# Performance work log

Hardware: AMD Instinct MI355X
Metric: run time of the kernel (lower is better)

Reference implementation:

```python
import jax, jax.numpy as jnp
import numpy as np

B, S, HID, NH = 4, 4096, 1024, 16
D = HID // NH
EPS = 1e-5


def setup_inputs() -> dict:
    key = jax.random.key(0)
    ks = jax.random.split(key, 8)
    x = jax.random.normal(ks[0], (B, S, HID), dtype=jnp.float32)
    sc = 0.03  # ~xavier for 1024x1024
    Wq = jax.random.normal(ks[1], (HID, HID), dtype=jnp.float32) * sc
    Wk = jax.random.normal(ks[2], (HID, HID), dtype=jnp.float32) * sc
    Wv = jax.random.normal(ks[3], (HID, HID), dtype=jnp.float32) * sc
    Wbeta = jax.random.normal(ks[4], (HID, NH), dtype=jnp.float32) * sc
    b_beta = jnp.full((NH,), 0.9, dtype=jnp.float32)  # init.constant_(0.9)
    Wo = jax.random.normal(ks[5], (HID, HID), dtype=jnp.float32) * sc
    b_o = jnp.zeros((HID,), dtype=jnp.float32)
    ln_g = jnp.ones((HID,), dtype=jnp.float32)
    ln_b = jnp.zeros((HID,), dtype=jnp.float32)
    return {"x": x, "Wq": Wq, "Wk": Wk, "Wv": Wv, "Wbeta": Wbeta,
            "b_beta": b_beta, "Wo": Wo, "b_o": b_o, "ln_g": ln_g, "ln_b": ln_b}


def _delta_scan(q, k, v, beta):
    # q,k,v: (B,S,NH,D); beta: (B,S,NH)
    # Faithful to torch einsum 'bik,bji->bjk' with broadcast over i:
    # update[b,h,:,k'] = k_t[b,h,k'] * sum_d v_t[b,h,d]  (same row repeated)
    vsum = v.sum(-1)  # (B,S,NH)
    qs = jnp.moveaxis(q, 1, 0)       # (S,B,NH,D)
    ks_ = jnp.moveaxis(k, 1, 0)
    vs = jnp.moveaxis(vsum, 1, 0)    # (S,B,NH)
    bs = jnp.moveaxis(beta, 1, 0)    # (S,B,NH)

    def step(h, inp):
        q_t, k_t, vsum_t, beta_t = inp
        h = h * beta_t[..., None, None]
        h = h + (k_t * vsum_t[..., None])[:, :, None, :]  # broadcast over rows
        o_t = jnp.einsum('bhj,bhjk->bhk', q_t, h)
        return h, o_t

    h0 = jnp.zeros((q.shape[0], q.shape[2], D, D), dtype=q.dtype)
    _, o = jax.lax.scan(step, h0, (qs, ks_, vs, bs))
    return jnp.moveaxis(o, 0, 1)  # (B,S,NH,D)


def reference(x, Wq, Wk, Wv, Wbeta, b_beta, Wo, b_o, ln_g, ln_b):
    b, s, hid = x.shape
    residual = x
    q = (x @ Wq).reshape(b, s, NH, D)
    k = (x @ Wk).reshape(b, s, NH, D)
    v = (x @ Wv).reshape(b, s, NH, D)
    beta = jax.nn.sigmoid(x @ Wbeta + b_beta)  # (B,S,NH)
    o = _delta_scan(q, k, v, beta).reshape(b, s, hid)
    out = o @ Wo + b_o  # dropout is identity in eval
    y = residual + out
    mu = y.mean(-1, keepdims=True)
    var = ((y - mu) ** 2).mean(-1, keepdims=True)
    return ln_g * (y - mu) * jax.lax.rsqrt(var + EPS) + ln_b
```

## Files before the change

kernel.cpp:

```cpp
#include <hip/hip_runtime.h>
#include <hip/hip_bf16.h>

typedef unsigned short u16;
typedef unsigned int   u32;
typedef u32 __attribute__((address_space(1))) gas_u32;
typedef u32 __attribute__((address_space(3))) las_u32;
typedef __bf16 bf16x8 __attribute__((ext_vector_type(8)));
typedef float  f32x4  __attribute__((ext_vector_type(4)));

constexpr int BATCH = 4, SEQ = 4096, HID = 1024, NH = 16, DH = 64;
constexpr int M  = BATCH * SEQ;
constexpr int KD = HID;

__device__ __forceinline__ u16 f2bf(float f) {
  __hip_bfloat16 h = __float2bfloat16(f);
  u16 u; __builtin_memcpy(&u, &h, 2); return u;
}
__device__ __forceinline__ float bf2f(u16 u) {
  u32 x = ((u32)u) << 16; float f; __builtin_memcpy(&f, &x, 4); return f;
}


__global__ __launch_bounds__(256) void transpose_cast(const float* __restrict__ Wk,
                                                      const float* __restrict__ Wo,
                                                      u16* __restrict__ WkT,
                                                      u16* __restrict__ WoT) {
  __shared__ float tile[32][33];
  const float* src = blockIdx.z ? Wo : Wk;
  u16* dst = blockIdx.z ? WoT : WkT;
  int bx = blockIdx.x * 32, by = blockIdx.y * 32;
  int tx = threadIdx.x & 31, ty = threadIdx.x >> 5;
#pragma unroll
  for (int i = 0; i < 4; i++)
    tile[ty + i * 8][tx] = src[(size_t)(by + ty + i * 8) * HID + bx + tx];
  __syncthreads();
#pragma unroll
  for (int i = 0; i < 4; i++)
    dst[(size_t)(bx + ty + i * 8) * HID + by + tx] = f2bf(tile[tx][ty + i * 8]);
}

__global__ __launch_bounds__(256) void build_wsum(const float* __restrict__ Wq,
                                                  const float* __restrict__ Wv,
                                                  const float* __restrict__ Wbeta,
                                                  u16* __restrict__ WsT) {
  int tid = blockIdx.x * 256 + threadIdx.x;
  int c = tid >> 10, kk = tid & 1023;
  float s = 0.f;
  if (c < 16)      { for (int d = 0; d < DH; d++) s += Wq[(size_t)kk * HID + c * DH + d]; }
  else if (c < 32) { for (int d = 0; d < DH; d++) s += Wv[(size_t)kk * HID + (c - 16) * DH + d]; }
  else if (c < 48) { s = Wbeta[(size_t)kk * NH + (c - 32)]; }
  WsT[(size_t)c * HID + kk] = f2bf(s);
}

__global__ __launch_bounds__(256) void skinny_part(
    const float* __restrict__ x, const u16* __restrict__ Bt,
    float* __restrict__ pq, float* __restrict__ pv, float* __restrict__ pb,
    u16* __restrict__ xb) {
  constexpr int BM = 64, BK = 64, KC = 256;
  __shared__ u16 As[BM * BK];
  __shared__ u16 Bs[64 * BK];
  const int tid = threadIdx.x, wave = tid >> 6, lane = tid & 63;
  const int bm = (int)blockIdx.x >> 2, kc = (int)blockIdx.x & 3;
  const int k0 = kc * KC;
  const int r16 = lane & 15, hi = lane >> 4;
  const int rsub = lane >> 3, csub = (lane & 7) * 8;
  f32x4 acc[4] = {};
  const float* Ab = x + (size_t)bm * BM * KD;
  u16* xbb = xb + (size_t)bm * BM * KD;

  for (int kt = k0; kt < k0 + KC; kt += BK) {
#pragma unroll
    for (int i = 0; i < 2; i++) {
      int slot = wave * 2 + i;
      const u16* g = Bt + (size_t)(slot * 8 + rsub) * KD + kt + csub;
      __builtin_amdgcn_global_load_lds((const gas_u32*)g, (las_u32*)(Bs + slot * 512), 16, 0, 0);
    }
#pragma unroll
    for (int p = 0; p < 2; p++) {
      const int row = p * 32 + (tid >> 3);
      const int c8 = (tid & 7) * 8;
      const float4 u0 = *(const float4*)(Ab + (size_t)row * KD + kt + c8);
      const float4 u1 = *(const float4*)(Ab + (size_t)row * KD + kt + c8 + 4);
      uint4 w;
      w.x = (u32)f2bf(u0.x) | ((u32)f2bf(u0.y) << 16);
      w.y = (u32)f2bf(u0.z) | ((u32)f2bf(u0.w) << 16);
      w.z = (u32)f2bf(u1.x) | ((u32)f2bf(u1.y) << 16);
      w.w = (u32)f2bf(u1.z) | ((u32)f2bf(u1.w) << 16);
      *(uint4*)(As + row * BK + c8) = w;
      *(uint4*)(xbb + (size_t)row * KD + kt + c8) = w;
    }
    __syncthreads();
#pragma unroll
    for (int kk = 0; kk < 2; kk++) {
      bf16x8 af = *(const bf16x8*)(As + (wave * 16 + r16) * BK + kk * 32 + hi * 8);
#pragma unroll
      for (int fn = 0; fn < 4; fn++) {
        bf16x8 bfr = *(const bf16x8*)(Bs + (fn * 16 + r16) * BK + kk * 32 + hi * 8);
        acc[fn] = __builtin_amdgcn_mfma_f32_16x16x32_bf16(af, bfr, acc[fn], 0, 0, 0);
      }
    }
    __syncthreads();
  }

  const size_t kcoff = (size_t)kc * 64 * SEQ;
#pragma unroll
  for (int fn = 0; fn < 4; fn++) {
    const int col = fn * 16 + r16;
#pragma unroll
    for (int j = 0; j < 4; j++) {
      const int row = bm * BM + wave * 16 + hi * 4 + j;
      const int b = row >> 12, t = row & 4095;
      float v = acc[fn][j];
      if (col < 16)      pq[kcoff + ((size_t)(b * 16 + col)) * SEQ + t] = v;
      else if (col < 32) pv[kcoff + ((size_t)(b * 16 + col - 16)) * SEQ + t] = v;
      else if (col < 48) pb[kcoff + ((size_t)(b * 16 + col - 32)) * SEQ + t] = v;
    }
  }
}


__device__ __forceinline__ void stage_quarter(const u16* __restrict__ Gk,
                                              int q, u16* lds_tile, int tid, int wave) {
  const int row = q * 64 + (tid >> 3);
  const int s = tid & 7;
  const u16* g = Gk + (size_t)row * KD + (size_t)((s ^ (row & 7)) << 3);
  u16* l = lds_tile + q * 4096 + wave * 512;
  __builtin_amdgcn_global_load_lds((const gas_u32*)g, (las_u32*)l, 16, 0, 0);
}

__device__ __forceinline__ const bf16x8* lds_frag(const u16* lds_tile, int row, int cg) {
  return (const bf16x8*)(lds_tile + ((size_t)row << 6) + (size_t)((cg ^ (row & 7)) << 3));
}

template <int EPI>
__global__ __launch_bounds__(512) void gemm256(
    const u16* __restrict__ A, const u16* __restrict__ Bt, int N,
    u16* __restrict__ Cb, const u16* __restrict__ xres, const float* __restrict__ bias) {
  constexpr int BK = 64, NT = KD / BK;
  __shared__ u16 lds[2][2][16384];
  const int tid = threadIdx.x, wave = tid >> 6, lane = tid & 63;
  const int wm = wave >> 2, wn = wave & 3;
  const int r16 = lane & 15, hi = lane >> 4;
  const int bid = (int)blockIdx.x;
  const int bm = (bid & 7) + 8 * (bid >> 5);
  const int bn = (bid >> 3) & 3;
  const u16* Abase = A + (size_t)bm * 256 * KD;
  const u16* Bbase = Bt + (size_t)bn * 256 * KD;

  f32x4 acc[8][4] = {};

  {
    u16* la = &lds[0][0][0]; u16* lb = &lds[0][1][0];
    stage_quarter(Abase, 0, la, tid, wave);
    stage_quarter(Abase, 2, la, tid, wave);
    stage_quarter(Bbase, 0, lb, tid, wave);
    stage_quarter(Bbase, 1, lb, tid, wave);
    stage_quarter(Bbase, 2, lb, tid, wave);
    stage_quarter(Bbase, 3, lb, tid, wave);
    stage_quarter(Abase, 1, la, tid, wave);
    stage_quarter(Abase, 3, la, tid, wave);
  }
  asm volatile("s_waitcnt vmcnt(2)" ::: "memory");
  __builtin_amdgcn_s_barrier();

  for (int kt = 0; kt < NT - 1; ++kt) {
    const int cur = kt & 1;
    const u16* la = &lds[cur][0][0];
    const u16* lb = &lds[cur][1][0];
    u16* na = &lds[cur ^ 1][0][0];
    u16* nb = &lds[cur ^ 1][1][0];
    const u16* An = Abase + (kt + 1) * BK;
    const u16* Bn = Bbase + (kt + 1) * BK;

    stage_quarter(An, 0, na, tid, wave);
    stage_quarter(An, 2, na, tid, wave);
    bf16x8 bF[4][2], aF0[4][2];
#pragma unroll
    for (int kk = 0; kk < 2; ++kk) {
#pragma unroll
      for (int f = 0; f < 4; ++f)
        aF0[f][kk] = *lds_frag(la, wm * 128 + f * 16 + r16, kk * 4 + hi);
#pragma unroll
      for (int g = 0; g < 4; ++g)
        bF[g][kk] = *lds_frag(lb, wn * 64 + g * 16 + r16, kk * 4 + hi);
    }
    stage_quarter(Bn, 0, nb, tid, wave);
    stage_quarter(Bn, 1, nb, tid, wave);
    __builtin_amdgcn_s_setprio(1);
#pragma unroll
    for (int kk = 0; kk < 2; ++kk)
#pragma unroll
      for (int f = 0; f < 4; ++f)
#pragma unroll
        for (int g = 0; g < 4; ++g)
          acc[f][g] = __builtin_amdgcn_mfma_f32_16x16x32_bf16(
              aF0[f][kk], bF[g][kk], acc[f][g], 0, 0, 0);
    __builtin_amdgcn_s_setprio(0);
    asm volatile("s_waitcnt vmcnt(4)" ::: "memory");
    __builtin_amdgcn_s_barrier();

    stage_quarter(Bn, 2, nb, tid, wave);
    stage_quarter(Bn, 3, nb, tid, wave);
    bf16x8 aF1[4][2];
#pragma unroll
    for (int kk = 0; kk < 2; ++kk)
#pragma unroll
      for (int f = 0; f < 4; ++f)
        aF1[f][kk] = *lds_frag(la, wm * 128 + 64 + f * 16 + r16, kk * 4 + hi);
    stage_quarter(An, 1, na, tid, wave);
    stage_quarter(An, 3, na, tid, wave);
    __builtin_amdgcn_s_setprio(1);
#pragma unroll
    for (int kk = 0; kk < 2; ++kk)
#pragma unroll
      for (int f = 0; f < 4; ++f)
#pragma unroll
        for (int g = 0; g < 4; ++g)
          acc[4 + f][g] = __builtin_amdgcn_mfma_f32_16x16x32_bf16(
              aF1[f][kk], bF[g][kk], acc[4 + f][g], 0, 0, 0);
    __builtin_amdgcn_s_setprio(0);
    asm volatile("s_waitcnt vmcnt(2)" ::: "memory");
    __builtin_amdgcn_s_barrier();
  }

  {
    const u16* la = &lds[(NT - 1) & 1][0][0];
    const u16* lb = &lds[(NT - 1) & 1][1][0];
    bf16x8 bF[4][2], aF0[4][2];
#pragma unroll
    for (int kk = 0; kk < 2; ++kk) {
#pragma unroll
      for (int f = 0; f < 4; ++f)
        aF0[f][kk] = *lds_frag(la, wm * 128 + f * 16 + r16, kk * 4 + hi);
#pragma unroll
      for (int g = 0; g < 4; ++g)
        bF[g][kk] = *lds_frag(lb, wn * 64 + g * 16 + r16, kk * 4 + hi);
    }
    __builtin_amdgcn_s_setprio(1);
#pragma unroll
    for (int kk = 0; kk < 2; ++kk)
#pragma unroll
      for (int f = 0; f < 4; ++f)
#pragma unroll
        for (int g = 0; g < 4; ++g)
          acc[f][g] = __builtin_amdgcn_mfma_f32_16x16x32_bf16(
              aF0[f][kk], bF[g][kk], acc[f][g], 0, 0, 0);
    __builtin_amdgcn_s_setprio(0);
    asm volatile("s_waitcnt vmcnt(0)" ::: "memory");
    __builtin_amdgcn_s_barrier();
    bf16x8 aF1[4][2];
#pragma unroll
    for (int kk = 0; kk < 2; ++kk)
#pragma unroll
      for (int f = 0; f < 4; ++f)
        aF1[f][kk] = *lds_frag(la, wm * 128 + 64 + f * 16 + r16, kk * 4 + hi);
    __builtin_amdgcn_s_setprio(1);
#pragma unroll
    for (int kk = 0; kk < 2; ++kk)
#pragma unroll
      for (int f = 0; f < 4; ++f)
#pragma unroll
        for (int g = 0; g < 4; ++g)
          acc[4 + f][g] = __builtin_amdgcn_mfma_f32_16x16x32_bf16(
              aF1[f][kk], bF[g][kk], acc[4 + f][g], 0, 0, 0);
    __builtin_amdgcn_s_setprio(0);
  }

#pragma unroll
  for (int fm = 0; fm < 8; ++fm) {
#pragma unroll
    for (int fn = 0; fn < 4; ++fn) {
      const int col = bn * 256 + wn * 64 + fn * 16 + r16;
#pragma unroll
      for (int j = 0; j < 4; ++j) {
        const int row = bm * 256 + wm * 128 + fm * 16 + hi * 4 + j;
        float v = acc[fm][fn][j];
        if constexpr (EPI == 2) v += bf2f(xres[(size_t)row * N + col]) + bias[col];
        Cb[(size_t)row * N + col] = f2bf(v);
      }
    }
  }
}


__global__ __launch_bounds__(256) void scan_chunks(const u16* __restrict__ kbuf,
                                                   const float* __restrict__ pv,
                                                   const float* __restrict__ pb,
                                                   const float* __restrict__ bbeta,
                                                   float* __restrict__ Pbuf,
                                                   float* __restrict__ Rloc) {
  constexpr size_t STR = (size_t)64 * SEQ;
  const int wave = threadIdx.x >> 6, lane = threadIdx.x & 63;
  const int gid = blockIdx.x * 4 + wave;
  const int seq = gid >> 6, chunk = gid & 63;
  const int b = seq >> 4, h = seq & 15;
  const int t0 = chunk * 64;
  const size_t idx = (size_t)seq * SEQ + t0 + lane;
  const float zb = pb[idx] + pb[idx + STR] + pb[idx + 2 * STR] + pb[idx + 3 * STR] + bbeta[h];
  const float bet = 1.f / (1.f + __expf(-zb));
  const float vs  = pv[idx] + pv[idx + STR] + pv[idx + 2 * STR] + pv[idx + 3 * STR];
  const u16* kp = kbuf + ((size_t)(b * SEQ + t0)) * HID + h * DH + lane;
  float r = 0.f, P = 1.f;
#pragma unroll
  for (int tt = 0; tt < 64; tt += 8) {
    u16 kr[8];
#pragma unroll
    for (int j = 0; j < 8; j++) kr[j] = kp[(size_t)(tt + j) * HID];
#pragma unroll
    for (int j = 0; j < 8; j++) {
      float bt = __shfl(bet, tt + j);
      float vt = __shfl(vs, tt + j);
      r = fmaf(r, bt, bf2f(kr[j]) * vt);
      P *= bt;
    }
  }
  Rloc[(size_t)gid * 64 + lane] = r;
  if (lane == 0) Pbuf[gid] = P;
}

__global__ __launch_bounds__(64) void scan_prefix(const float* __restrict__ Pbuf,
                                                  const float* __restrict__ Rloc,
                                                  float* __restrict__ Rin) {
  const int seq = blockIdx.x, lane = threadIdx.x;
  const float* pp = Pbuf + seq * 64;
  const float* rl = Rloc + (size_t)seq * 64 * 64 + lane;
  float* ri = Rin + (size_t)seq * 64 * 64 + lane;
  float rin = 0.f;
#pragma unroll
  for (int c0 = 0; c0 < 64; c0 += 8) {
    float P[8], L[8];
#pragma unroll
    for (int j = 0; j < 8; j++) { P[j] = pp[c0 + j]; L[j] = rl[(size_t)(c0 + j) * 64]; }
#pragma unroll
    for (int j = 0; j < 8; j++) {
      ri[(size_t)(c0 + j) * 64] = rin;
      rin = fmaf(P[j], rin, L[j]);
    }
  }
}

__global__ __launch_bounds__(256) void scan_apply(const u16* __restrict__ kbuf,
                                                  const float* __restrict__ pq,
                                                  const float* __restrict__ pv,
                                                  const float* __restrict__ pb,
                                                  const float* __restrict__ bbeta,
                                                  const float* __restrict__ Rin,
                                                  u16* __restrict__ obuf) {
  constexpr size_t STR = (size_t)64 * SEQ;
  const int wave = threadIdx.x >> 6, lane = threadIdx.x & 63;
  const int gid = blockIdx.x * 4 + wave;
  const int seq = gid >> 6, chunk = gid & 63;
  const int b = seq >> 4, h = seq & 15;
  const int t0 = chunk * 64;
  const size_t idx = (size_t)seq * SEQ + t0 + lane;
  const float zb = pb[idx] + pb[idx + STR] + pb[idx + 2 * STR] + pb[idx + 3 * STR] + bbeta[h];
  const float bet = 1.f / (1.f + __expf(-zb));
  const float vs  = pv[idx] + pv[idx + STR] + pv[idx + 2 * STR] + pv[idx + 3 * STR];
  const float qs  = pq[idx] + pq[idx + STR] + pq[idx + 2 * STR] + pq[idx + 3 * STR];
  const u16* kp = kbuf + ((size_t)(b * SEQ + t0)) * HID + h * DH + lane;
  u16* op = obuf + ((size_t)(b * SEQ + t0)) * HID + h * DH + lane;
  float r = Rin[(size_t)gid * 64 + lane];
#pragma unroll
  for (int tt = 0; tt < 64; tt += 8) {
    u16 kr[8];
#pragma unroll
    for (int j = 0; j < 8; j++) kr[j] = kp[(size_t)(tt + j) * HID];
#pragma unroll
    for (int j = 0; j < 8; j++) {
      float bt = __shfl(bet, tt + j);
      float vt = __shfl(vs, tt + j);
      float qt = __shfl(qs, tt + j);
      r = fmaf(r, bt, bf2f(kr[j]) * vt);
      op[(size_t)(tt + j) * HID] = f2bf(qt * r);
    }
  }
}

__global__ __launch_bounds__(256) void ln_kernel(const u16* __restrict__ y,
                                                 const float* __restrict__ g,
                                                 const float* __restrict__ bt,
                                                 float* __restrict__ out) {
  const int row = blockIdx.x;
  const u16* yr = y + (size_t)row * HID;
  const int t = threadIdx.x;
  ushort4 u = *(const ushort4*)(yr + t * 4);
  float v0 = bf2f(u.x), v1 = bf2f(u.y), v2 = bf2f(u.z), v3 = bf2f(u.w);
  float s  = v0 + v1 + v2 + v3;
  float ss = v0 * v0 + v1 * v1 + v2 * v2 + v3 * v3;
#pragma unroll
  for (int m = 1; m < 64; m <<= 1) { s += __shfl_xor(s, m); ss += __shfl_xor(ss, m); }
  __shared__ float red[8];
  const int wave = t >> 6, lane = t & 63;
  if (lane == 0) { red[wave] = s; red[4 + wave] = ss; }
  __syncthreads();
  float st  = red[0] + red[1] + red[2] + red[3];
  float sst = red[4] + red[5] + red[6] + red[7];
  float mu  = st * (1.f / 1024.f);
  float var = sst * (1.f / 1024.f) - mu * mu;
  float inv = rsqrtf(var + 1e-5f);
  const int c = t * 4;
  float4 o;
  o.x = g[c + 0] * ((v0 - mu) * inv) + bt[c + 0];
  o.y = g[c + 1] * ((v1 - mu) * inv) + bt[c + 1];
  o.z = g[c + 2] * ((v2 - mu) * inv) + bt[c + 2];
  o.w = g[c + 3] * ((v3 - mu) * inv) + bt[c + 3];
  *(float4*)(out + (size_t)row * HID + c) = o;
}

extern "C" void kernel_launch(void* const* d_in, const int* in_sizes, int n_in,
                              void* d_out, int out_size, void* d_ws, size_t ws_size,
                              hipStream_t stream) {
  const float* x     = (const float*)d_in[0];
  const float* Wq    = (const float*)d_in[1];
  const float* Wk    = (const float*)d_in[2];
  const float* Wv    = (const float*)d_in[3];
  const float* Wbeta = (const float*)d_in[4];
  const float* bbeta = (const float*)d_in[5];
  const float* Wo    = (const float*)d_in[6];
  const float* b_o   = (const float*)d_in[7];
  const float* ln_g  = (const float*)d_in[8];
  const float* ln_b  = (const float*)d_in[9];
  float* out = (float*)d_out;

  char* ws = (char*)d_ws;
  size_t off = 0;
  auto alloc = [&](size_t bytes) {
    char* p = ws + off; off += (bytes + 255) & ~(size_t)255; return p;
  };
  u16* xb   = (u16*)alloc((size_t)M * HID * 2);
  u16* kbuf = (u16*)alloc((size_t)M * HID * 2);
  u16* obuf = (u16*)alloc((size_t)M * HID * 2);
  u16* WkT  = (u16*)alloc((size_t)HID * HID * 2);
  u16* WoT  = (u16*)alloc((size_t)HID * HID * 2);
  u16* WsT  = (u16*)alloc((size_t)64 * HID * 2);
  float* pq = (float*)alloc((size_t)4 * 64 * SEQ * 4);
  float* pv = (float*)alloc((size_t)4 * 64 * SEQ * 4);
  float* pb = (float*)alloc((size_t)4 * 64 * SEQ * 4);
  float* Pbuf = (float*)alloc((size_t)4096 * 4);
  float* Rloc = (float*)alloc((size_t)4096 * 64 * 4);
  float* Rin  = (float*)alloc((size_t)4096 * 64 * 4);
  u16* ybuf = kbuf;

  transpose_cast<<<dim3(32, 32, 2), 256, 0, stream>>>(Wk, Wo, WkT, WoT);
  build_wsum<<<256, 256, 0, stream>>>(Wq, Wv, Wbeta, WsT);

  skinny_part<<<(M / 64) * 4, 256, 0, stream>>>(x, WsT, pq, pv, pb, xb);

  gemm256<0><<<(M / 256) * (HID / 256), 512, 0, stream>>>(
      xb, WkT, HID, kbuf, nullptr, nullptr);

  scan_chunks<<<1024, 256, 0, stream>>>(kbuf, pv, pb, bbeta, Pbuf, Rloc);
  scan_prefix<<<64, 64, 0, stream>>>(Pbuf, Rloc, Rin);
  scan_apply<<<1024, 256, 0, stream>>>(kbuf, pq, pv, pb, bbeta, Rin, obuf);

  gemm256<2><<<(M / 256) * (HID / 256), 512, 0, stream>>>(
      obuf, WoT, HID, ybuf, xb, b_o);

  ln_kernel<<<M, 256, 0, stream>>>(ybuf, ln_g, ln_b, out);
}
```

Baseline: 150.6 us.

## Deepen GEMM global-to-LDS prefetch to keep two K-tiles in flight

The prologue now stages both the first and second K-tiles into the two LDS buffers. Inside the loop, each iteration finishes the remaining A quarters of tile kt+1 and then issues loads for tile kt+2 into the buffer currently being consumed, once its first half has been read. The aim is more memory-level parallelism and less exposed global-load latency, with loads waited at vmcnt(8) instead of 4/2. The peeled final iteration is folded into the loop with conditional waits. The cost is tighter reuse of the current buffer and more delicate vmcnt accounting, which could cause races or stalls if the quarter-to-row mapping or the counts are off.

```diff
diff --git a/kernel.cpp b/kernel.cpp
--- a/kernel.cpp
+++ b/kernel.cpp
@@ -150,30 +150,38 @@
   f32x4 acc[8][4] = {};
 
   {
-    u16* la = &lds[0][0][0]; u16* lb = &lds[0][1][0];
-    stage_quarter(Abase, 0, la, tid, wave);
-    stage_quarter(Abase, 2, la, tid, wave);
-    stage_quarter(Bbase, 0, lb, tid, wave);
-    stage_quarter(Bbase, 1, lb, tid, wave);
-    stage_quarter(Bbase, 2, lb, tid, wave);
-    stage_quarter(Bbase, 3, lb, tid, wave);
-    stage_quarter(Abase, 1, la, tid, wave);
-    stage_quarter(Abase, 3, la, tid, wave);
-  }
-  asm volatile("s_waitcnt vmcnt(2)" ::: "memory");
+    u16* la0 = &lds[0][0][0]; u16* lb0 = &lds[0][1][0];
+    stage_quarter(Abase, 0, la0, tid, wave);
+    stage_quarter(Abase, 2, la0, tid, wave);
+    stage_quarter(Bbase, 0, lb0, tid, wave);
+    stage_quarter(Bbase, 1, lb0, tid, wave);
+    stage_quarter(Bbase, 2, lb0, tid, wave);
+    stage_quarter(Bbase, 3, lb0, tid, wave);
+    stage_quarter(Abase, 1, la0, tid, wave);
+    stage_quarter(Abase, 3, la0, tid, wave);
+    const u16* A1 = Abase + BK; const u16* B1 = Bbase + BK;
+    u16* la1 = &lds[1][0][0]; u16* lb1 = &lds[1][1][0];
+    stage_quarter(A1, 0, la1, tid, wave);
+    stage_quarter(A1, 2, la1, tid, wave);
+    stage_quarter(B1, 0, lb1, tid, wave);
+    stage_quarter(B1, 1, lb1, tid, wave);
+    stage_quarter(B1, 2, lb1, tid, wave);
+    stage_quarter(B1, 3, lb1, tid, wave);
+  }
+  asm volatile("s_waitcnt vmcnt(8)" ::: "memory");
   __builtin_amdgcn_s_barrier();
 
-  for (int kt = 0; kt < NT - 1; ++kt) {
+  for (int kt = 0; kt < NT; ++kt) {
     const int cur = kt & 1;
     const u16* la = &lds[cur][0][0];
     const u16* lb = &lds[cur][1][0];
-    u16* na = &lds[cur ^ 1][0][0];
-    u16* nb = &lds[cur ^ 1][1][0];
-    const u16* An = Abase + (kt + 1) * BK;
-    const u16* Bn = Bbase + (kt + 1) * BK;
-
-    stage_quarter(An, 0, na, tid, wave);
-    stage_quarter(An, 2, na, tid, wave);
+
+    if (kt + 1 < NT) {
+      const u16* An1 = Abase + (kt + 1) * BK;
+      u16* na = &lds[cur ^ 1][0][0];
+      stage_quarter(An1, 1, na, tid, wave);
+      stage_quarter(An1, 3, na, tid, wave);
+    }
     bf16x8 bF[4][2], aF0[4][2];
 #pragma unroll
     for (int kk = 0; kk < 2; ++kk) {
@@ -184,8 +192,6 @@
       for (int g = 0; g < 4; ++g)
         bF[g][kk] = *lds_frag(lb, wn * 64 + g * 16 + r16, kk * 4 + hi);
     }
-    stage_quarter(Bn, 0, nb, tid, wave);
-    stage_quarter(Bn, 1, nb, tid, wave);
     __builtin_amdgcn_s_setprio(1);
 #pragma unroll
     for (int kk = 0; kk < 2; ++kk)
@@ -196,19 +202,28 @@
           acc[f][g] = __builtin_amdgcn_mfma_f32_16x16x32_bf16(
               aF0[f][kk], bF[g][kk], acc[f][g], 0, 0, 0);
     __builtin_amdgcn_s_setprio(0);
-    asm volatile("s_waitcnt vmcnt(4)" ::: "memory");
+    if (kt < NT - 1)      { asm volatile("s_waitcnt vmcnt(8)" ::: "memory"); }
+    else                  { asm volatile("s_waitcnt vmcnt(0)" ::: "memory"); }
     __builtin_amdgcn_s_barrier();
 
-    stage_quarter(Bn, 2, nb, tid, wave);
-    stage_quarter(Bn, 3, nb, tid, wave);
+    if (kt + 2 < NT) {
+      const u16* An2 = Abase + (kt + 2) * BK;
+      const u16* Bn2 = Bbase + (kt + 2) * BK;
+      u16* ca = &lds[cur][0][0];
+      u16* cb = &lds[cur][1][0];
+      stage_quarter(An2, 0, ca, tid, wave);
+      stage_quarter(An2, 2, ca, tid, wave);
+      stage_quarter(Bn2, 0, cb, tid, wave);
+      stage_quarter(Bn2, 1, cb, tid, wave);
+      stage_quarter(Bn2, 2, cb, tid, wave);
+      stage_quarter(Bn2, 3, cb, tid, wave);
+    }
     bf16x8 aF1[4][2];
 #pragma unroll
     for (int kk = 0; kk < 2; ++kk)
 #pragma unroll
       for (int f = 0; f < 4; ++f)
         aF1[f][kk] = *lds_frag(la, wm * 128 + 64 + f * 16 + r16, kk * 4 + hi);
-    stage_quarter(An, 1, na, tid, wave);
-    stage_quarter(An, 3, na, tid, wave);
     __builtin_amdgcn_s_setprio(1);
 #pragma unroll
     for (int kk = 0; kk < 2; ++kk)
@@ -219,51 +234,8 @@
           acc[4 + f][g] = __builtin_amdgcn_mfma_f32_16x16x32_bf16(
               aF1[f][kk], bF[g][kk], acc[4 + f][g], 0, 0, 0);
     __builtin_amdgcn_s_setprio(0);
-    asm volatile("s_waitcnt vmcnt(2)" ::: "memory");
-    __builtin_amdgcn_s_barrier();
-  }
-
-  {
-    const u16* la = &lds[(NT - 1) & 1][0][0];
-    const u16* lb = &lds[(NT - 1) & 1][1][0];
-    bf16x8 bF[4][2], aF0[4][2];
-#pragma unroll
-    for (int kk = 0; kk < 2; ++kk) {
-#pragma unroll
-      for (int f = 0; f < 4; ++f)
-        aF0[f][kk] = *lds_frag(la, wm * 128 + f * 16 + r16, kk * 4 + hi);
-#pragma unroll
-      for (int g = 0; g < 4; ++g)
-        bF[g][kk] = *lds_frag(lb, wn * 64 + g * 16 + r16, kk * 4 + hi);
-    }
-    __builtin_amdgcn_s_setprio(1);
-#pragma unroll
-    for (int kk = 0; kk < 2; ++kk)
-#pragma unroll
-      for (int f = 0; f < 4; ++f)
-#pragma unroll
-        for (int g = 0; g < 4; ++g)
-          acc[f][g] = __builtin_amdgcn_mfma_f32_16x16x32_bf16(
-              aF0[f][kk], bF[g][kk], acc[f][g], 0, 0, 0);
-    __builtin_amdgcn_s_setprio(0);
-    asm volatile("s_waitcnt vmcnt(0)" ::: "memory");
-    __builtin_amdgcn_s_barrier();
-    bf16x8 aF1[4][2];
-#pragma unroll
-    for (int kk = 0; kk < 2; ++kk)
-#pragma unroll
-      for (int f = 0; f < 4; ++f)
-        aF1[f][kk] = *lds_frag(la, wm * 128 + 64 + f * 16 + r16, kk * 4 + hi);
-    __builtin_amdgcn_s_setprio(1);
-#pragma unroll
-    for (int kk = 0; kk < 2; ++kk)
-#pragma unroll
-      for (int f = 0; f < 4; ++f)
-#pragma unroll
-        for (int g = 0; g < 4; ++g)
-          acc[4 + f][g] = __builtin_amdgcn_mfma_f32_16x16x32_bf16(
-              aF1[f][kk], bF[g][kk], acc[4 + f][g], 0, 0, 0);
-    __builtin_amdgcn_s_setprio(0);
+    if (kt < NT - 2)      { asm volatile("s_waitcnt vmcnt(8)" ::: "memory"); __builtin_amdgcn_s_barrier(); }
+    else if (kt == NT - 2){ asm volatile("s_waitcnt vmcnt(2)" ::: "memory"); __builtin_amdgcn_s_barrier(); }
   }
 
 #pragma unroll
```

After: 150.7 us. No clear change (+0.1%).
